# Kernel tuning notes

Measured on AMD Instinct MI355X. Metric: run time of the kernel, lower is better.

Reference implementation:

```python
import jax, jax.numpy as jnp
import numpy as np

EPS = 1e-4
NEG_BIAS = 0.01


def setup_inputs() -> dict:
    key = jax.random.key(0)
    ks = jax.random.split(key, 9)
    B, L, D_MODEL, HALF = 4, 4096, 2048, 32
    return {
        "u": jax.random.normal(ks[0], (B, L, D_MODEL), dtype=jnp.float32),
        "Lambda_unconstrained_re": jax.random.normal(ks[1], (HALF,), dtype=jnp.float32) * 0.1 - 1.0,
        "Lambda_im": jax.random.normal(ks[2], (HALF,), dtype=jnp.float32) * 3.0,
        "B_re": jax.random.normal(ks[3], (HALF, D_MODEL), dtype=jnp.float32) * 0.02,
        "B_im": jax.random.normal(ks[4], (HALF, D_MODEL), dtype=jnp.float32) * 0.02,
        "C_re": jax.random.normal(ks[5], (D_MODEL, HALF), dtype=jnp.float32) * 0.05,
        "C_im": jax.random.normal(ks[6], (D_MODEL, HALF), dtype=jnp.float32) * 0.05,
        "D": jax.random.normal(ks[7], (D_MODEL,), dtype=jnp.float32) * 0.1,
        "log_Delta": jax.random.uniform(ks[8], (2 * HALF,), minval=-3.0, maxval=-1.0, dtype=jnp.float32),
    }


def reference(u, Lambda_unconstrained_re, Lambda_im, B_re, B_im, C_re, C_im, D, log_Delta):
    half = Lambda_im.shape[0]
    # Constrained continuous-time eigenvalues: Re < 0 via softplus (inverse of init formula)
    lam_re = -(jax.nn.softplus(Lambda_unconstrained_re) + EPS + NEG_BIAS)
    Lam = lam_re + 1j * Lambda_im                      # [half]
    Delta = jnp.exp(log_Delta[:half])                  # per-state timestep
    # ZOH discretization
    Lam_bar = jnp.exp(Lam * Delta)                     # [half]
    B_tilde = (B_re + 1j * B_im).astype(jnp.complex64) # [half, d]
    B_bar = ((Lam_bar - 1.0) / Lam)[:, None] * B_tilde # [half, d]
    # Input projection: Bu[b,l,n]
    Bu = jnp.einsum("bld,nd->bln", u.astype(jnp.complex64), B_bar)
    a = jnp.broadcast_to(Lam_bar, Bu.shape)

    def op(e1, e2):
        a1, b1 = e1
        a2, b2 = e2
        return (a1 * a2, a2 * b1 + b2)

    # Parallel associative scan of x_t = Lam_bar * x_{t-1} + Bu_t along time axis
    _, xs = jax.lax.associative_scan(op, (a, Bu), axis=1)  # [b, l, half]
    C_tilde = (C_re + 1j * C_im).astype(jnp.complex64)     # [d, half]
    # Conjugate symmetry -> 2 * real part, plus skip connection D * u
    y = 2.0 * jnp.real(jnp.einsum("bln,dn->bld", xs, C_tilde)) + D * u
    return y
```

## Files before the change

kernel.cpp:

```cpp
#include <hip/hip_runtime.h>
#include <math.h>

#define M_ROWS 16384
#define DM     2048
#define NJ     64
#define L_SEQ  4096

typedef __bf16 bf16x8 __attribute__((ext_vector_type(8)));
typedef float  f32x4  __attribute__((ext_vector_type(4)));

constexpr size_t OB_BBART = 0;
constexpr size_t OB_CCT   = 256 * 1024;
constexpr size_t OB_BUT   = 512 * 1024;
constexpr size_t OB_XST   = 512 * 1024 + 4194304;

static __device__ __forceinline__ unsigned short f2bf(float f) {
  unsigned int u = __float_as_uint(f);
  u = (u + 0x7fffu + ((u >> 16) & 1u)) >> 16;
  return (unsigned short)u;
}

static __device__ __forceinline__ bf16x8 cvt8(float4 a, float4 b) {
  bf16x8 r;
  r[0] = (__bf16)a.x; r[1] = (__bf16)a.y; r[2] = (__bf16)a.z; r[3] = (__bf16)a.w;
  r[4] = (__bf16)b.x; r[5] = (__bf16)b.y; r[6] = (__bf16)b.z; r[7] = (__bf16)b.w;
  return r;
}

__global__ void k_prep(const float* __restrict__ lam_ur, const float* __restrict__ lam_im,
                       const float* __restrict__ log_dt,
                       const float* __restrict__ Bre, const float* __restrict__ Bim,
                       const float* __restrict__ Cre, const float* __restrict__ Cim,
                       unsigned short* __restrict__ bbarT, unsigned short* __restrict__ ccT) {
  const int idx = blockIdx.x * 256 + threadIdx.x;
  {
    const int j = idx >> 11, d = idx & 2047, n = j >> 1;
    float x = lam_ur[n];
    float sp = (x > 20.f) ? x : log1pf(expf(x));
    float lre = -(sp + 1.0e-4f + 0.01f);
    float lim = lam_im[n];
    float dt = expf(log_dt[n]);
    float er = expf(lre * dt);
    float Are = er * cosf(lim * dt);
    float Aim = er * sinf(lim * dt);
    float den = lre * lre + lim * lim;
    float cre = ((Are - 1.f) * lre + Aim * lim) / den;
    float cim = (Aim * lre - (Are - 1.f) * lim) / den;
    float br = Bre[n * DM + d], bi = Bim[n * DM + d];
    float v = (j & 1) ? (cre * bi + cim * br) : (cre * br - cim * bi);
    bbarT[(size_t)j * DM + d] = f2bf(v);
  }
  {
    const int j = idx & 63, d = idx >> 6, n = j >> 1;
    float v = (j & 1) ? (-2.f * Cim[d * 32 + n]) : (2.f * Cre[d * 32 + n]);
    ccT[(size_t)d * NJ + j] = f2bf(v);
  }
}

__global__ __launch_bounds__(256) void k_bu(const float* __restrict__ u,
                                            const unsigned short* __restrict__ bbarT,
                                            float* __restrict__ bu_t) {
  const int t = threadIdx.x;
  const int wave = t >> 6, lane = t & 63;
  const int rs = wave & 1;
  const int jh = wave >> 1;
  const int m0 = blockIdx.x * 32 + rs * 16;
  const int l15 = lane & 15, kq8 = (lane >> 4) * 8;
  const float* up = u + (size_t)(m0 + l15) * DM + kq8;
  const unsigned short* bp0 = bbarT + (size_t)(jh * 32 + l15) * DM + kq8;
  const unsigned short* bp1 = bp0 + (size_t)16 * DM;
  f32x4 acc0 = {0.f, 0.f, 0.f, 0.f}, acc1 = {0.f, 0.f, 0.f, 0.f};
  float4 cv0 = *(const float4*)(up);
  float4 cv1 = *(const float4*)(up + 4);
  bf16x8 cb0 = *(const bf16x8*)(bp0);
  bf16x8 cb1 = *(const bf16x8*)(bp1);
#pragma unroll 4
  for (int k0 = 32; k0 < DM; k0 += 32) {
    float4 nv0 = *(const float4*)(up + k0);
    float4 nv1 = *(const float4*)(up + k0 + 4);
    bf16x8 nb0 = *(const bf16x8*)(bp0 + k0);
    bf16x8 nb1 = *(const bf16x8*)(bp1 + k0);
    bf16x8 a = cvt8(cv0, cv1);
    acc0 = __builtin_amdgcn_mfma_f32_16x16x32_bf16(a, cb0, acc0, 0, 0, 0);
    acc1 = __builtin_amdgcn_mfma_f32_16x16x32_bf16(a, cb1, acc1, 0, 0, 0);
    cv0 = nv0; cv1 = nv1; cb0 = nb0; cb1 = nb1;
  }
  {
    bf16x8 a = cvt8(cv0, cv1);
    acc0 = __builtin_amdgcn_mfma_f32_16x16x32_bf16(a, cb0, acc0, 0, 0, 0);
    acc1 = __builtin_amdgcn_mfma_f32_16x16x32_bf16(a, cb1, acc1, 0, 0, 0);
  }
  const int j0 = jh * 32 + l15;
  const int orow = m0 + (lane >> 4) * 4;
  *(f32x4*)&bu_t[(size_t)j0 * M_ROWS + orow] = acc0;
  *(f32x4*)&bu_t[(size_t)(j0 + 16) * M_ROWS + orow] = acc1;
}

__global__ __launch_bounds__(256) void k_scan(const float* __restrict__ bu_t,
                                              const float* __restrict__ lam_ur,
                                              const float* __restrict__ lam_im,
                                              const float* __restrict__ log_dt,
                                              unsigned short* __restrict__ xs_t) {
  __shared__ float sre[L_SEQ + 256], sim[L_SEQ + 256];
  __shared__ float2 P[256];
  const int n = blockIdx.x;
  const int b = blockIdx.y;
  const int t = threadIdx.x;
  float x = lam_ur[n];
  float sp = (x > 20.f) ? x : log1pf(expf(x));
  float lre = -(sp + 1.0e-4f + 0.01f);
  float lim = lam_im[n];
  float dt = expf(log_dt[n]);
  float er = expf(lre * dt);
  const float Are = er * cosf(lim * dt);
  const float Aim = er * sinf(lim * dt);
  const float* pr = bu_t + (size_t)(2 * n) * M_ROWS + (size_t)b * L_SEQ;
  const float* pi = bu_t + (size_t)(2 * n + 1) * M_ROWS + (size_t)b * L_SEQ;
#pragma unroll
  for (int i0 = 4 * t; i0 < L_SEQ; i0 += 1024) {
    float4 vr = *(const float4*)(pr + i0);
    float4 vi = *(const float4*)(pi + i0);
    const float rr[4] = {vr.x, vr.y, vr.z, vr.w};
    const float ii[4] = {vi.x, vi.y, vi.z, vi.w};
#pragma unroll
    for (int q = 0; q < 4; ++q) {
      int e = i0 + q, ee = e + (e >> 4);
      sre[ee] = rr[q];
      sim[ee] = ii[q];
    }
  }
  __syncthreads();
  float lre16[16], lim16[16];
  float xre = 0.f, xim = 0.f;
#pragma unroll
  for (int i = 0; i < 16; ++i) {
    float bre = sre[17 * t + i], bim = sim[17 * t + i];
    float nr = Are * xre - Aim * xim + bre;
    float ni = Are * xim + Aim * xre + bim;
    xre = nr; xim = ni;
    lre16[i] = nr; lim16[i] = ni;
  }
  float Mre = Are, Mim = Aim;
#pragma unroll
  for (int k = 0; k < 4; ++k) {
    float nr = Mre * Mre - Mim * Mim;
    float ni = 2.f * Mre * Mim;
    Mre = nr; Mim = ni;
  }
  float pre = xre, pim = xim;
  P[t] = make_float2(pre, pim);
  __syncthreads();
  float msre = Mre, msim = Mim;
  for (int s = 1; s < 256; s <<= 1) {
    float2 prev = (t >= s) ? P[t - s] : make_float2(0.f, 0.f);
    __syncthreads();
    pre += msre * prev.x - msim * prev.y;
    pim += msre * prev.y + msim * prev.x;
    P[t] = make_float2(pre, pim);
    float nr = msre * msre - msim * msim;
    float ni = 2.f * msre * msim;
    msre = nr; msim = ni;
    __syncthreads();
  }
  float2 E = (t == 0) ? make_float2(0.f, 0.f) : P[t - 1];
  float pwre = Are, pwim = Aim;
#pragma unroll
  for (int i = 0; i < 16; ++i) {
    sre[17 * t + i] = lre16[i] + pwre * E.x - pwim * E.y;
    sim[17 * t + i] = lim16[i] + pwre * E.y + pwim * E.x;
    float nr = pwre * Are - pwim * Aim;
    float ni = pwre * Aim + pwim * Are;
    pwre = nr; pwim = ni;
  }
  __syncthreads();
  unsigned int* xp = (unsigned int*)(xs_t + (size_t)b * L_SEQ * NJ + 2 * n);
  for (int i = t; i < L_SEQ; i += 256) {
    int p = i + (i >> 4);
    xp[(size_t)i * (NJ / 2)] = ((unsigned int)f2bf(sim[p]) << 16) | f2bf(sre[p]);
  }
}

__global__ __launch_bounds__(256) void k_out(const unsigned short* __restrict__ xs_t,
                                             const unsigned short* __restrict__ ccT,
                                             const float* __restrict__ u,
                                             const float* __restrict__ Dv,
                                             float* __restrict__ y) {
  __shared__ __align__(16) float Es[64][132];
  const int t = threadIdx.x;
  const int wave = t >> 6, lane = t & 63;
  const int m0 = blockIdx.x * 64;
  const int d0 = blockIdx.y * 128;
  const int l15 = lane & 15, kq8 = (lane >> 4) * 8;
  const unsigned short* ap = xs_t + (size_t)(m0 + wave * 16 + l15) * NJ;
  bf16x8 a0 = *(const bf16x8*)(ap + kq8);
  bf16x8 a1 = *(const bf16x8*)(ap + 32 + kq8);
  f32x4 acc[8];
#pragma unroll
  for (int c = 0; c < 8; ++c) acc[c] = (f32x4){0.f, 0.f, 0.f, 0.f};
#pragma unroll
  for (int c = 0; c < 8; ++c) {
    const unsigned short* cp = ccT + (size_t)(d0 + c * 16 + l15) * NJ + kq8;
    bf16x8 b0 = *(const bf16x8*)cp;
    bf16x8 b1 = *(const bf16x8*)(cp + 32);
    acc[c] = __builtin_amdgcn_mfma_f32_16x16x32_bf16(a0, b0, acc[c], 0, 0, 0);
    acc[c] = __builtin_amdgcn_mfma_f32_16x16x32_bf16(a1, b1, acc[c], 0, 0, 0);
  }
#pragma unroll
  for (int c = 0; c < 8; ++c)
#pragma unroll
    for (int i = 0; i < 4; ++i)
      Es[wave * 16 + (lane >> 4) * 4 + i][c * 16 + l15] = acc[c][i];
  __syncthreads();
#pragma unroll
  for (int p = 0; p < 8; ++p) {
    int idx = t + 256 * p;
    int row = idx >> 5;
    int c4 = (idx & 31) * 4;
    f32x4 e = *(const f32x4*)&Es[row][c4];
    const size_t off = (size_t)(m0 + row) * DM + d0 + c4;
    float4 uu = *(const float4*)&u[off];
    float4 dd = *(const float4*)&Dv[d0 + c4];
    float4 o;
    o.x = e[0] + dd.x * uu.x;
    o.y = e[1] + dd.y * uu.y;
    o.z = e[2] + dd.z * uu.z;
    o.w = e[3] + dd.w * uu.w;
    *(float4*)&y[off] = o;
  }
}

extern "C" void kernel_launch(void* const* d_in, const int* in_sizes, int n_in,
                              void* d_out, int out_size, void* d_ws, size_t ws_size,
                              hipStream_t stream) {
  const float* u      = (const float*)d_in[0];
  const float* lam_ur = (const float*)d_in[1];
  const float* lam_im = (const float*)d_in[2];
  const float* B_re   = (const float*)d_in[3];
  const float* B_im   = (const float*)d_in[4];
  const float* C_re   = (const float*)d_in[5];
  const float* C_im   = (const float*)d_in[6];
  const float* Dv     = (const float*)d_in[7];
  const float* log_dt = (const float*)d_in[8];
  float* y = (float*)d_out;
  char* ws = (char*)d_ws;

  unsigned short* bbarT = (unsigned short*)(ws + OB_BBART);
  unsigned short* ccT   = (unsigned short*)(ws + OB_CCT);
  float*          bu_t  = (float*)(ws + OB_BUT);
  unsigned short* xs_t  = (unsigned short*)(ws + OB_XST);

  k_prep<<<512, 256, 0, stream>>>(lam_ur, lam_im, log_dt, B_re, B_im, C_re, C_im, bbarT, ccT);
  k_bu<<<M_ROWS / 32, 256, 0, stream>>>(u, bbarT, bu_t);
  k_scan<<<dim3(32, 4), 256, 0, stream>>>(bu_t, lam_ur, lam_im, log_dt, xs_t);
  k_out<<<dim3(M_ROWS / 64, DM / 128), 256, 0, stream>>>(xs_t, ccT, u, Dv, y);
}
```

Before: 321.2 us.

## Split-K input projection, deeper prefetch, and reuse a bf16 copy of u for skip

The input projection now splits its reduction over two K halves in separate blocks to double the grid, writing two partial results that the scan kernel sums when loading. Its load pipeline is restructured into a four-stage register prefetch. While converting u to bf16 it also writes a bf16 copy of u, which the output kernel reads instead of the fp32 u for the D*u skip term, halving that read traffic. The trade-offs are extra writes of the bf16 u copy and the partial sums, plus lower precision in the skip term.

```diff
diff --git a/kernel.cpp b/kernel.cpp
--- a/kernel.cpp
+++ b/kernel.cpp
@@ -5,6 +5,7 @@
 #define DM     2048
 #define NJ     64
 #define L_SEQ  4096
+#define KH     1024
 
 typedef __bf16 bf16x8 __attribute__((ext_vector_type(8)));
 typedef float  f32x4  __attribute__((ext_vector_type(4)));
@@ -12,7 +13,8 @@
 constexpr size_t OB_BBART = 0;
 constexpr size_t OB_CCT   = 256 * 1024;
 constexpr size_t OB_BUT   = 512 * 1024;
-constexpr size_t OB_XST   = 512 * 1024 + 4194304;
+constexpr size_t OB_XST   = 512 * 1024 + 8u * 1024 * 1024;
+constexpr size_t OB_UBF   = OB_XST + 2u * 1024 * 1024;
 
 static __device__ __forceinline__ unsigned short f2bf(float f) {
   unsigned int u = __float_as_uint(f);
@@ -59,41 +61,54 @@
 
 __global__ __launch_bounds__(256) void k_bu(const float* __restrict__ u,
                                             const unsigned short* __restrict__ bbarT,
-                                            float* __restrict__ bu_t) {
+                                            float* __restrict__ bu_t,
+                                            unsigned short* __restrict__ ubf) {
   const int t = threadIdx.x;
   const int wave = t >> 6, lane = t & 63;
   const int rs = wave & 1;
   const int jh = wave >> 1;
   const int m0 = blockIdx.x * 32 + rs * 16;
+  const int ks = blockIdx.y;
+  const int kb = ks * KH;
   const int l15 = lane & 15, kq8 = (lane >> 4) * 8;
-  const float* up = u + (size_t)(m0 + l15) * DM + kq8;
-  const unsigned short* bp0 = bbarT + (size_t)(jh * 32 + l15) * DM + kq8;
+  const float* up = u + (size_t)(m0 + l15) * DM + kb + kq8;
+  const unsigned short* bp0 = bbarT + (size_t)(jh * 32 + l15) * DM + kb + kq8;
   const unsigned short* bp1 = bp0 + (size_t)16 * DM;
+  unsigned short* wp = ubf + (size_t)(m0 + l15) * DM + kb + kq8;
   f32x4 acc0 = {0.f, 0.f, 0.f, 0.f}, acc1 = {0.f, 0.f, 0.f, 0.f};
-  float4 cv0 = *(const float4*)(up);
-  float4 cv1 = *(const float4*)(up + 4);
-  bf16x8 cb0 = *(const bf16x8*)(bp0);
-  bf16x8 cb1 = *(const bf16x8*)(bp1);
-#pragma unroll 4
-  for (int k0 = 32; k0 < DM; k0 += 32) {
-    float4 nv0 = *(const float4*)(up + k0);
-    float4 nv1 = *(const float4*)(up + k0 + 4);
-    bf16x8 nb0 = *(const bf16x8*)(bp0 + k0);
-    bf16x8 nb1 = *(const bf16x8*)(bp1 + k0);
-    bf16x8 a = cvt8(cv0, cv1);
-    acc0 = __builtin_amdgcn_mfma_f32_16x16x32_bf16(a, cb0, acc0, 0, 0, 0);
-    acc1 = __builtin_amdgcn_mfma_f32_16x16x32_bf16(a, cb1, acc1, 0, 0, 0);
-    cv0 = nv0; cv1 = nv1; cb0 = nb0; cb1 = nb1;
-  }
-  {
-    bf16x8 a = cvt8(cv0, cv1);
-    acc0 = __builtin_amdgcn_mfma_f32_16x16x32_bf16(a, cb0, acc0, 0, 0, 0);
-    acc1 = __builtin_amdgcn_mfma_f32_16x16x32_bf16(a, cb1, acc1, 0, 0, 0);
-  }
+  float4 v0_0, v1_0, v0_1, v1_1, v0_2, v1_2, v0_3, v1_3;
+  bf16x8 b0_0, b1_0, b0_1, b1_1, b0_2, b1_2, b0_3, b1_3;
+#define LOADS(S, K)                                  \
+  do {                                               \
+    v0_##S = *(const float4*)(up + (K));             \
+    v1_##S = *(const float4*)(up + (K) + 4);         \
+    b0_##S = *(const bf16x8*)(bp0 + (K));            \
+    b1_##S = *(const bf16x8*)(bp1 + (K));            \
+  } while (0)
+#define CONSUME(S, K)                                                        \
+  do {                                                                       \
+    bf16x8 a = cvt8(v0_##S, v1_##S);                                         \
+    if (jh == 0) *(bf16x8*)(wp + (K)) = a;                                   \
+    acc0 = __builtin_amdgcn_mfma_f32_16x16x32_bf16(a, b0_##S, acc0, 0, 0, 0);\
+    acc1 = __builtin_amdgcn_mfma_f32_16x16x32_bf16(a, b1_##S, acc1, 0, 0, 0);\
+  } while (0)
+  LOADS(0, 0); LOADS(1, 32); LOADS(2, 64); LOADS(3, 96);
+  int k0 = 0;
+#pragma unroll 1
+  for (int it = 0; it < (KH / 128) - 1; ++it, k0 += 128) {
+    CONSUME(0, k0);      LOADS(0, k0 + 128);
+    CONSUME(1, k0 + 32); LOADS(1, k0 + 160);
+    CONSUME(2, k0 + 64); LOADS(2, k0 + 192);
+    CONSUME(3, k0 + 96); LOADS(3, k0 + 224);
+  }
+  CONSUME(0, k0); CONSUME(1, k0 + 32); CONSUME(2, k0 + 64); CONSUME(3, k0 + 96);
+#undef LOADS
+#undef CONSUME
   const int j0 = jh * 32 + l15;
   const int orow = m0 + (lane >> 4) * 4;
-  *(f32x4*)&bu_t[(size_t)j0 * M_ROWS + orow] = acc0;
-  *(f32x4*)&bu_t[(size_t)(j0 + 16) * M_ROWS + orow] = acc1;
+  float* bo = bu_t + (size_t)ks * NJ * M_ROWS;
+  *(f32x4*)&bo[(size_t)j0 * M_ROWS + orow] = acc0;
+  *(f32x4*)&bo[(size_t)(j0 + 16) * M_ROWS + orow] = acc1;
 }
 
 __global__ __launch_bounds__(256) void k_scan(const float* __restrict__ bu_t,
@@ -114,14 +129,18 @@
   float er = expf(lre * dt);
   const float Are = er * cosf(lim * dt);
   const float Aim = er * sinf(lim * dt);
-  const float* pr = bu_t + (size_t)(2 * n) * M_ROWS + (size_t)b * L_SEQ;
-  const float* pi = bu_t + (size_t)(2 * n + 1) * M_ROWS + (size_t)b * L_SEQ;
+  const float* pr0 = bu_t + (size_t)(2 * n) * M_ROWS + (size_t)b * L_SEQ;
+  const float* pi0 = bu_t + (size_t)(2 * n + 1) * M_ROWS + (size_t)b * L_SEQ;
+  const float* pr1 = pr0 + (size_t)NJ * M_ROWS;
+  const float* pi1 = pi0 + (size_t)NJ * M_ROWS;
 #pragma unroll
   for (int i0 = 4 * t; i0 < L_SEQ; i0 += 1024) {
-    float4 vr = *(const float4*)(pr + i0);
-    float4 vi = *(const float4*)(pi + i0);
-    const float rr[4] = {vr.x, vr.y, vr.z, vr.w};
-    const float ii[4] = {vi.x, vi.y, vi.z, vi.w};
+    float4 va = *(const float4*)(pr0 + i0);
+    float4 vb = *(const float4*)(pr1 + i0);
+    float4 wa = *(const float4*)(pi0 + i0);
+    float4 wb = *(const float4*)(pi1 + i0);
+    const float rr[4] = {va.x + vb.x, va.y + vb.y, va.z + vb.z, va.w + vb.w};
+    const float ii[4] = {wa.x + wb.x, wa.y + wb.y, wa.z + wb.z, wa.w + wb.w};
 #pragma unroll
     for (int q = 0; q < 4; ++q) {
       int e = i0 + q, ee = e + (e >> 4);
@@ -182,7 +201,7 @@
 
 __global__ __launch_bounds__(256) void k_out(const unsigned short* __restrict__ xs_t,
                                              const unsigned short* __restrict__ ccT,
-                                             const float* __restrict__ u,
+                                             const unsigned short* __restrict__ ubf,
                                              const float* __restrict__ Dv,
                                              float* __restrict__ y) {
   __shared__ __align__(16) float Es[64][132];
@@ -218,13 +237,13 @@
     int c4 = (idx & 31) * 4;
     f32x4 e = *(const f32x4*)&Es[row][c4];
     const size_t off = (size_t)(m0 + row) * DM + d0 + c4;
-    float4 uu = *(const float4*)&u[off];
+    ushort4 ub = *(const ushort4*)&ubf[off];
     float4 dd = *(const float4*)&Dv[d0 + c4];
     float4 o;
-    o.x = e[0] + dd.x * uu.x;
-    o.y = e[1] + dd.y * uu.y;
-    o.z = e[2] + dd.z * uu.z;
-    o.w = e[3] + dd.w * uu.w;
+    o.x = e[0] + dd.x * __uint_as_float((unsigned int)ub.x << 16);
+    o.y = e[1] + dd.y * __uint_as_float((unsigned int)ub.y << 16);
+    o.z = e[2] + dd.z * __uint_as_float((unsigned int)ub.z << 16);
+    o.w = e[3] + dd.w * __uint_as_float((unsigned int)ub.w << 16);
     *(float4*)&y[off] = o;
   }
 }
@@ -248,9 +267,10 @@
   unsigned short* ccT   = (unsigned short*)(ws + OB_CCT);
   float*          bu_t  = (float*)(ws + OB_BUT);
   unsigned short* xs_t  = (unsigned short*)(ws + OB_XST);
+  unsigned short* ubf   = (unsigned short*)(ws + OB_UBF);
 
   k_prep<<<512, 256, 0, stream>>>(lam_ur, lam_im, log_dt, B_re, B_im, C_re, C_im, bbarT, ccT);
-  k_bu<<<M_ROWS / 32, 256, 0, stream>>>(u, bbarT, bu_t);
+  k_bu<<<dim3(M_ROWS / 32, 2), 256, 0, stream>>>(u, bbarT, bu_t, ubf);
   k_scan<<<dim3(32, 4), 256, 0, stream>>>(bu_t, lam_ur, lam_im, log_dt, xs_t);
-  k_out<<<dim3(M_ROWS / 64, DM / 128), 256, 0, stream>>>(xs_t, ccT, u, Dv, y);
-}
+  k_out<<<dim3(M_ROWS / 64, DM / 128), 256, 0, stream>>>(xs_t, ccT, ubf, Dv, y);
+}
```

Result: slower. 356.1 us (+10.9%).

## Split-K the input projection and stage u tiles in LDS via direct loads

Applied to the files above, without the earlier changes.

The Bu GEMM now splits the 2048-wide reduction into two halves across a second grid dimension, doubling block count, and writes two partial outputs that the scan kernel sums on load. Each block stages 32x128 tiles of u into swizzled LDS using global_load_lds, so the two waves sharing rows no longer each fetch u from global memory. The cost is extra workspace and traffic for the second partial buffer, plus block-level barriers per k-step.

```diff
diff --git a/kernel.cpp b/kernel.cpp
--- a/kernel.cpp
+++ b/kernel.cpp
@@ -5,6 +5,7 @@
 #define DM     2048
 #define NJ     64
 #define L_SEQ  4096
+#define KH     1024
 
 typedef __bf16 bf16x8 __attribute__((ext_vector_type(8)));
 typedef float  f32x4  __attribute__((ext_vector_type(4)));
@@ -12,7 +13,10 @@
 constexpr size_t OB_BBART = 0;
 constexpr size_t OB_CCT   = 256 * 1024;
 constexpr size_t OB_BUT   = 512 * 1024;
-constexpr size_t OB_XST   = 512 * 1024 + 4194304;
+constexpr size_t OB_XST   = 512 * 1024 + 8u * 1024 * 1024;
+
+#define AS1C(p) ((const __attribute__((address_space(1))) unsigned int*)(p))
+#define AS3(p)  ((__attribute__((address_space(3))) unsigned int*)(p))
 
 static __device__ __forceinline__ unsigned short f2bf(float f) {
   unsigned int u = __float_as_uint(f);
@@ -60,40 +64,49 @@
 __global__ __launch_bounds__(256) void k_bu(const float* __restrict__ u,
                                             const unsigned short* __restrict__ bbarT,
                                             float* __restrict__ bu_t) {
+  __shared__ __align__(16) float Ut[32 * 128];
   const int t = threadIdx.x;
   const int wave = t >> 6, lane = t & 63;
   const int rs = wave & 1;
   const int jh = wave >> 1;
-  const int m0 = blockIdx.x * 32 + rs * 16;
+  const int m0 = blockIdx.x * 32;
+  const int ks = blockIdx.y;
   const int l15 = lane & 15, kq8 = (lane >> 4) * 8;
-  const float* up = u + (size_t)(m0 + l15) * DM + kq8;
-  const unsigned short* bp0 = bbarT + (size_t)(jh * 32 + l15) * DM + kq8;
+  const int srow = wave * 2 + (lane >> 5);
+  const int sslot = lane & 31;
+  const int r = rs * 16 + l15;
+  const unsigned short* bp0 = bbarT + (size_t)(jh * 32 + l15) * DM + ks * KH + kq8;
   const unsigned short* bp1 = bp0 + (size_t)16 * DM;
   f32x4 acc0 = {0.f, 0.f, 0.f, 0.f}, acc1 = {0.f, 0.f, 0.f, 0.f};
-  float4 cv0 = *(const float4*)(up);
-  float4 cv1 = *(const float4*)(up + 4);
-  bf16x8 cb0 = *(const bf16x8*)(bp0);
-  bf16x8 cb1 = *(const bf16x8*)(bp1);
-#pragma unroll 4
-  for (int k0 = 32; k0 < DM; k0 += 32) {
-    float4 nv0 = *(const float4*)(up + k0);
-    float4 nv1 = *(const float4*)(up + k0 + 4);
-    bf16x8 nb0 = *(const bf16x8*)(bp0 + k0);
-    bf16x8 nb1 = *(const bf16x8*)(bp1 + k0);
-    bf16x8 a = cvt8(cv0, cv1);
-    acc0 = __builtin_amdgcn_mfma_f32_16x16x32_bf16(a, cb0, acc0, 0, 0, 0);
-    acc1 = __builtin_amdgcn_mfma_f32_16x16x32_bf16(a, cb1, acc1, 0, 0, 0);
-    cv0 = nv0; cv1 = nv1; cb0 = nb0; cb1 = nb1;
-  }
-  {
-    bf16x8 a = cvt8(cv0, cv1);
-    acc0 = __builtin_amdgcn_mfma_f32_16x16x32_bf16(a, cb0, acc0, 0, 0, 0);
-    acc1 = __builtin_amdgcn_mfma_f32_16x16x32_bf16(a, cb1, acc1, 0, 0, 0);
+#pragma unroll 1
+  for (int step = 0; step < KH / 128; ++step) {
+    const int k0 = ks * KH + step * 128;
+#pragma unroll
+    for (int p = 0; p < 4; ++p) {
+      const int row = p * 8 + srow;
+      const float* src = u + (size_t)(m0 + row) * DM + k0 + ((sslot ^ (row & 7)) << 2);
+      __builtin_amdgcn_global_load_lds(AS1C(src), AS3(&Ut[p * 1024 + wave * 256]),
+                                       16, 0, 0);
+    }
+    __syncthreads();
+#pragma unroll
+    for (int c = 0; c < 4; ++c) {
+      const int f4a = c * 8 + (kq8 >> 2);
+      float4 va = *(const float4*)&Ut[(r * 32 + (f4a ^ (r & 7))) * 4];
+      float4 vb = *(const float4*)&Ut[(r * 32 + ((f4a + 1) ^ (r & 7))) * 4];
+      bf16x8 a = cvt8(va, vb);
+      bf16x8 b0 = *(const bf16x8*)(bp0 + step * 128 + c * 32);
+      bf16x8 b1 = *(const bf16x8*)(bp1 + step * 128 + c * 32);
+      acc0 = __builtin_amdgcn_mfma_f32_16x16x32_bf16(a, b0, acc0, 0, 0, 0);
+      acc1 = __builtin_amdgcn_mfma_f32_16x16x32_bf16(a, b1, acc1, 0, 0, 0);
+    }
+    __syncthreads();
   }
   const int j0 = jh * 32 + l15;
-  const int orow = m0 + (lane >> 4) * 4;
-  *(f32x4*)&bu_t[(size_t)j0 * M_ROWS + orow] = acc0;
-  *(f32x4*)&bu_t[(size_t)(j0 + 16) * M_ROWS + orow] = acc1;
+  const int orow = m0 + rs * 16 + (lane >> 4) * 4;
+  float* bo = bu_t + (size_t)ks * NJ * M_ROWS;
+  *(f32x4*)&bo[(size_t)j0 * M_ROWS + orow] = acc0;
+  *(f32x4*)&bo[(size_t)(j0 + 16) * M_ROWS + orow] = acc1;
 }
 
 __global__ __launch_bounds__(256) void k_scan(const float* __restrict__ bu_t,
@@ -114,14 +127,18 @@
   float er = expf(lre * dt);
   const float Are = er * cosf(lim * dt);
   const float Aim = er * sinf(lim * dt);
-  const float* pr = bu_t + (size_t)(2 * n) * M_ROWS + (size_t)b * L_SEQ;
-  const float* pi = bu_t + (size_t)(2 * n + 1) * M_ROWS + (size_t)b * L_SEQ;
+  const float* pr0 = bu_t + (size_t)(2 * n) * M_ROWS + (size_t)b * L_SEQ;
+  const float* pi0 = bu_t + (size_t)(2 * n + 1) * M_ROWS + (size_t)b * L_SEQ;
+  const float* pr1 = pr0 + (size_t)NJ * M_ROWS;
+  const float* pi1 = pi0 + (size_t)NJ * M_ROWS;
 #pragma unroll
   for (int i0 = 4 * t; i0 < L_SEQ; i0 += 1024) {
-    float4 vr = *(const float4*)(pr + i0);
-    float4 vi = *(const float4*)(pi + i0);
-    const float rr[4] = {vr.x, vr.y, vr.z, vr.w};
-    const float ii[4] = {vi.x, vi.y, vi.z, vi.w};
+    float4 va = *(const float4*)(pr0 + i0);
+    float4 vb = *(const float4*)(pr1 + i0);
+    float4 wa = *(const float4*)(pi0 + i0);
+    float4 wb = *(const float4*)(pi1 + i0);
+    const float rr[4] = {va.x + vb.x, va.y + vb.y, va.z + vb.z, va.w + vb.w};
+    const float ii[4] = {wa.x + wb.x, wa.y + wb.y, wa.z + wb.z, wa.w + wb.w};
 #pragma unroll
     for (int q = 0; q < 4; ++q) {
       int e = i0 + q, ee = e + (e >> 4);
@@ -250,7 +267,7 @@
   unsigned short* xs_t  = (unsigned short*)(ws + OB_XST);
 
   k_prep<<<512, 256, 0, stream>>>(lam_ur, lam_im, log_dt, B_re, B_im, C_re, C_im, bbarT, ccT);
-  k_bu<<<M_ROWS / 32, 256, 0, stream>>>(u, bbarT, bu_t);
+  k_bu<<<dim3(M_ROWS / 32, 2), 256, 0, stream>>>(u, bbarT, bu_t);
   k_scan<<<dim3(32, 4), 256, 0, stream>>>(bu_t, lam_ur, lam_im, log_dt, xs_t);
   k_out<<<dim3(M_ROWS / 64, DM / 128), 256, 0, stream>>>(xs_t, ccT, u, Dv, y);
 }
```

Result: faster. 309.7 us (-3.6%).
